# Performance work log

Hardware: AMD Instinct MI355X
Metric: run time of the kernel (lower is better)

Reference implementation:

```python
import jax, jax.numpy as jnp
import numpy as np

N_NODES = 100000


def setup_inputs() -> dict:
    key = jax.random.key(0)
    ks = jax.random.split(key, 8)
    IN, HID, OUT = 128, 128, 64
    E = 1600000
    x = jax.random.normal(ks[0], (N_NODES, IN), dtype=jnp.float32)
    edge_index = jax.random.randint(ks[1], (2, E), 0, N_NODES, dtype=jnp.int64)
    # PyG SAGEConv params: lin_l (applied to aggregated neighbors, with bias),
    # lin_r (root weight, no bias).
    def lin(k, fi, fo):
        return jax.random.normal(k, (fi, fo), dtype=jnp.float32) / np.sqrt(fi)
    Wl0 = lin(ks[2], IN, HID)
    bl0 = jnp.zeros((HID,), dtype=jnp.float32)
    Wr0 = lin(ks[3], IN, HID)
    Wl1 = lin(ks[4], HID, OUT)
    bl1 = jnp.zeros((OUT,), dtype=jnp.float32)
    Wr1 = lin(ks[5], HID, OUT)
    return {"x": x, "edge_index": edge_index,
            "Wl0": Wl0, "bl0": bl0, "Wr0": Wr0,
            "Wl1": Wl1, "bl1": bl1, "Wr1": Wr1}


def _sage_conv(h, src, dst, Wl, bl, Wr):
    # mean aggregation of source features onto target nodes
    summed = jax.ops.segment_sum(h[src], dst, num_segments=N_NODES)  # [N, d]
    cnt = jax.ops.segment_sum(jnp.ones((src.shape[0], 1), h.dtype), dst,
                              num_segments=N_NODES)                  # [N, 1]
    agg = summed / jnp.maximum(cnt, 1.0)
    return agg @ Wl + bl + h @ Wr


def reference(x, edge_index, Wl0, bl0, Wr0, Wl1, bl1, Wr1):
    src, dst = edge_index[0], edge_index[1]
    h = jax.nn.relu(_sage_conv(x, src, dst, Wl0, bl0, Wr0))
    # dropout is identity in eval mode (training=False)
    return _sage_conv(h, src, dst, Wl1, bl1, Wr1)
```

## Files before the change

### kernel.cpp

```cpp
#include <hip/hip_runtime.h>


typedef short short8 __attribute__((ext_vector_type(8)));
typedef float f32x4 __attribute__((ext_vector_type(4)));
typedef float f32x2 __attribute__((ext_vector_type(2)));

#define NBUCK 782
#define BCAP  3072
#define EPB   8192

static __device__ __forceinline__ unsigned short f2bf(float f) {
    union { float f; unsigned u; } c; c.f = f;
    unsigned u = c.u + 0x7fffu + ((c.u >> 16) & 1u);
    return (unsigned short)(u >> 16);
}
static __device__ __forceinline__ float bf2f(unsigned short b) {
    union { unsigned u; float f; } c; c.u = ((unsigned)b) << 16;
    return c.f;
}
static __device__ __forceinline__ float bf2f_s(short b) {
    return bf2f((unsigned short)b);
}

static __device__ __forceinline__ unsigned char f2fp8(float x) {
    union { float f; unsigned u; } c; c.f = x;
    unsigned s = (c.u >> 24) & 0x80u;
    float a = __builtin_fabsf(x);
    if (a < 0.015625f) {
        int m = (int)rintf(a * 512.0f);
        return (unsigned char)(s | (unsigned)m);
    }
    unsigned u = c.u + 0x7ffffu + ((c.u >> 20) & 1u);
    int e = (int)((u >> 23) & 0xff) - 120;
    unsigned m = (u >> 20) & 7u;
    if (e > 15) { e = 15; m = 6; }
    return (unsigned char)(s | (unsigned)(e << 3) | m);
}

static __device__ __forceinline__ void acc_fp8x4(unsigned w, float* a) {
#if __has_builtin(__builtin_amdgcn_cvt_pk_f32_fp8)
    f32x2 lo = __builtin_amdgcn_cvt_pk_f32_fp8((int)w, false);
    f32x2 hi = __builtin_amdgcn_cvt_pk_f32_fp8((int)w, true);
    a[0] += lo[0]; a[1] += lo[1]; a[2] += hi[0]; a[3] += hi[1];
#else
    #pragma unroll
    for (int j = 0; j < 4; ++j) {
        unsigned b = (w >> (8 * j)) & 0xffu;
        union { unsigned u; float f; } c;
        c.u = ((b & 0x80u) << 24) | ((b & 0x7fu) << 20);
        a[j] += c.f * 0x1p120f;
    }
#endif
}
static __device__ __forceinline__ void acc_row16(uint4 w, float* a) {
    acc_fp8x4(w.x, a + 0);  acc_fp8x4(w.y, a + 4);
    acc_fp8x4(w.z, a + 8);  acc_fp8x4(w.w, a + 12);
}

__global__ __launch_bounds__(256) void k_pack2(const float* __restrict__ Wl0,
        const float* __restrict__ Wr0, const float* __restrict__ Wl1,
        const float* __restrict__ Wr1, unsigned short* __restrict__ Wp0,
        unsigned short* __restrict__ Wp1) {
    int tid = blockIdx.x * 256 + threadIdx.x;
    const float *WA, *WB; int CA; unsigned short* Wp;
    if (tid < 4096) {
        WA = Wl0; WB = Wr0; CA = 128; Wp = Wp0;
    } else {
        tid -= 4096;
        if (tid >= 2048) return;
        WA = Wl1; WB = Wr1; CA = 64; Wp = Wp1;
    }
    int lane = tid & 63, kk = (tid >> 6) & 3, tg = tid >> 8;
    int l15 = lane & 15, quad = lane >> 4;
    int c = tg * 16 + l15;
    const float* W = (c < CA) ? WA : WB;
    int cc = (c < CA) ? c : c - CA;
    short8 v;
    #pragma unroll
    for (int j = 0; j < 8; ++j) {
        int k = kk * 32 + quad * 8 + j;
        v[j] = (short)f2bf(W[(size_t)k * CA + cc]);
    }
    *(short8*)(Wp + (size_t)tid * 8) = v;
}

__global__ __launch_bounds__(512) void k_gemm0_bucket(
        const float* __restrict__ X, const unsigned short* __restrict__ Wp,
        unsigned char* __restrict__ P0, unsigned short* __restrict__ Q0, int Nrows,
        const int* __restrict__ src, const int* __restrict__ dst,
        int* __restrict__ cursor, int* __restrict__ bregion,
        int E, int bucketBlocks) {
    const int t = threadIdx.x;
    if ((int)blockIdx.x >= bucketBlocks) {
        const int wave = t >> 6, lane = t & 63;
        const int sub = wave >> 2, wv = wave & 3;
        const int quad = lane >> 4, l15 = lane & 15;
        const int row0 = (blockIdx.x - bucketBlocks) * 64 + sub * 32;
        const int c0w = wv * 64;
        float4 xf[4][2][2];
        #pragma unroll
        for (int mt = 0; mt < 2; ++mt) {
            int row = row0 + mt * 16 + l15;
            if (row > Nrows - 1) row = Nrows - 1;
            const float* xp = X + (size_t)row * 128 + quad * 8;
            #pragma unroll
            for (int kk = 0; kk < 4; ++kk) {
                xf[kk][mt][0] = *(const float4*)(xp + kk * 32);
                xf[kk][mt][1] = *(const float4*)(xp + kk * 32 + 4);
            }
        }
        short8 a[4][2];
        #pragma unroll
        for (int kk = 0; kk < 4; ++kk)
            #pragma unroll
            for (int mt = 0; mt < 2; ++mt) {
                float4 f0 = xf[kk][mt][0], f1 = xf[kk][mt][1];
                short8 v;
                v[0] = (short)f2bf(f0.x); v[1] = (short)f2bf(f0.y);
                v[2] = (short)f2bf(f0.z); v[3] = (short)f2bf(f0.w);
                v[4] = (short)f2bf(f1.x); v[5] = (short)f2bf(f1.y);
                v[6] = (short)f2bf(f1.z); v[7] = (short)f2bf(f1.w);
                a[kk][mt] = v;
            }
        f32x4 acc[2][4];
        #pragma unroll
        for (int mt = 0; mt < 2; ++mt)
            #pragma unroll
            for (int tt = 0; tt < 4; ++tt) acc[mt][tt] = (f32x4){0.f, 0.f, 0.f, 0.f};
        #pragma unroll
        for (int kk = 0; kk < 4; ++kk) {
            short8 b[4];
            #pragma unroll
            for (int tt = 0; tt < 4; ++tt) {
                int tg = (c0w >> 4) + tt;
                b[tt] = *(const short8*)(Wp + ((size_t)(tg * 4 + kk) * 64 + lane) * 8);
            }
            #pragma unroll
            for (int mt = 0; mt < 2; ++mt)
                #pragma unroll
                for (int tt = 0; tt < 4; ++tt)
                    acc[mt][tt] = __builtin_amdgcn_mfma_f32_16x16x32_bf16(
                        a[kk][mt], b[tt], acc[mt][tt], 0, 0, 0);
        }
        #pragma unroll
        for (int mt = 0; mt < 2; ++mt)
            #pragma unroll
            for (int r = 0; r < 4; ++r) {
                int row = row0 + mt * 16 + quad * 4 + r;
                if (row < Nrows) {
                    if (c0w < 128) {
                        #pragma unroll
                        for (int tt = 0; tt < 4; ++tt)
                            P0[(size_t)row * 128 + c0w + tt * 16 + l15] =
                                f2fp8(acc[mt][tt][r]);
                    } else {
                        #pragma unroll
                        for (int tt = 0; tt < 4; ++tt)
                            Q0[(size_t)row * 128 + (c0w - 128) + tt * 16 + l15] =
                                f2bf(acc[mt][tt][r]);
                    }
                }
            }
        return;
    }
    __shared__ int hist[NBUCK];
    __shared__ int basel[NBUCK];
    int bid = blockIdx.x;
    for (int i = t; i < NBUCK; i += 512) hist[i] = 0;
    __syncthreads();
    int e0 = bid * EPB + t * 16;
    if (e0 + 16 <= E) {
        #pragma unroll
        for (int q = 0; q < 4; ++q) {
            int4 v = *(const int4*)(dst + e0 + q * 4);
            atomicAdd(&hist[v.x >> 7], 1);
            atomicAdd(&hist[v.y >> 7], 1);
            atomicAdd(&hist[v.z >> 7], 1);
            atomicAdd(&hist[v.w >> 7], 1);
        }
    } else {
        for (int j = 0; j < 16; ++j)
            if (e0 + j < E) atomicAdd(&hist[dst[e0 + j] >> 7], 1);
    }
    __syncthreads();
    for (int i = t; i < NBUCK; i += 512) {
        int c = hist[i];
        basel[i] = (c > 0) ? atomicAdd(&cursor[i], c) : 0;
    }
    __syncthreads();
    for (int i = t; i < NBUCK; i += 512) hist[i] = 0;
    __syncthreads();
    if (e0 + 16 <= E) {
        #pragma unroll
        for (int q = 0; q < 4; ++q) {
            int4 dv = *(const int4*)(dst + e0 + q * 4);
            int4 sv = *(const int4*)(src + e0 + q * 4);
            int dd[4] = {dv.x, dv.y, dv.z, dv.w};
            int ss[4] = {sv.x, sv.y, sv.z, sv.w};
            #pragma unroll
            for (int j = 0; j < 4; ++j) {
                int b = dd[j] >> 7;
                int r = atomicAdd(&hist[b], 1);
                bregion[(size_t)b * BCAP + basel[b] + r] = ss[j] | ((dd[j] & 127) << 20);
            }
        }
    } else {
        for (int j = 0; j < 16; ++j) {
            if (e0 + j < E) {
                int dd = dst[e0 + j], ss = src[e0 + j];
                int b = dd >> 7;
                int r = atomicAdd(&hist[b], 1);
                bregion[(size_t)b * BCAP + basel[b] + r] = ss | ((dd & 127) << 20);
            }
        }
    }
}

__global__ __launch_bounds__(256) void k_csr(const int* __restrict__ cursor,
                                             const int* __restrict__ bregion,
                                             int* __restrict__ rowptr,
                                             int* __restrict__ csr, int Nn) {
    __shared__ int words[BCAP];
    __shared__ int hist[128], sc[128], rank[128];
    __shared__ int red[256];
    int b = blockIdx.x, t = threadIdx.x;
    int part = 0;
    for (int i = t; i < b; i += 256) part += cursor[i];
    red[t] = part;
    if (t < 128) { hist[t] = 0; rank[t] = 0; }
    __syncthreads();
    #pragma unroll
    for (int off = 128; off > 0; off >>= 1) {
        if (t < off) red[t] += red[t + off];
        __syncthreads();
    }
    int gbase = red[0];
    int cnt = cursor[b];
    for (int i = t; i < cnt; i += 256) {
        int w = bregion[(size_t)b * BCAP + i];
        words[i] = w;
        atomicAdd(&hist[w >> 20], 1);
    }
    __syncthreads();
    if (t < 128) sc[t] = hist[t];
    __syncthreads();
    #pragma unroll
    for (int off = 1; off < 128; off <<= 1) {
        int x = 0;
        if (t < 128 && t >= off) x = sc[t - off];
        __syncthreads();
        if (t < 128) sc[t] += x;
        __syncthreads();
    }
    if (t < 128) sc[t] -= hist[t];
    __syncthreads();
    if (t < 128) {
        int node = b * 128 + t;
        if (node <= Nn) rowptr[node] = gbase + sc[t];
    }
    for (int i = t; i < cnt; i += 256) {
        int w = words[i];
        int d7 = w >> 20;
        int r = atomicAdd(&rank[d7], 1);
        csr[gbase + sc[d7] + r] = w & 0xFFFFF;
    }
}

__global__ __launch_bounds__(256) void k_agg0_gemm1(
        const unsigned char* __restrict__ P0,
        const unsigned short* __restrict__ Q0,
        const int* __restrict__ rowptr, const int* __restrict__ csr,
        const float* __restrict__ bl0,
        const unsigned short* __restrict__ Wp,
        unsigned char* __restrict__ P1, unsigned short* __restrict__ Q1,
        int Nn) {
    __shared__ unsigned short ht[32 * 128];
    const int t = threadIdx.x;
    const int wave = t >> 6, lane = t & 63;
    {
        int g = lane >> 3, l7 = lane & 7;
        int nloc = wave * 8 + g;
        int n = blockIdx.x * 32 + nloc;
        bool live = (n < Nn);
        int st = 0, dg = 0;
        if (live) { st = rowptr[n]; dg = rowptr[n + 1] - st; }
        float acc[16] = {};
        int e = 0;
        for (; e + 4 <= dg; e += 4) {
            int s0 = csr[st + e];
            int s1 = csr[st + e + 1];
            int s2 = csr[st + e + 2];
            int s3 = csr[st + e + 3];
            uint4 w0 = *(const uint4*)(P0 + (size_t)s0 * 128 + l7 * 16);
            uint4 w1 = *(const uint4*)(P0 + (size_t)s1 * 128 + l7 * 16);
            uint4 w2 = *(const uint4*)(P0 + (size_t)s2 * 128 + l7 * 16);
            uint4 w3 = *(const uint4*)(P0 + (size_t)s3 * 128 + l7 * 16);
            acc_row16(w0, acc);
            acc_row16(w1, acc);
            acc_row16(w2, acc);
            acc_row16(w3, acc);
        }
        for (; e < dg; ++e) {
            int s0 = csr[st + e];
            uint4 w0 = *(const uint4*)(P0 + (size_t)s0 * 128 + l7 * 16);
            acc_row16(w0, acc);
        }
        short8 o0 = (short8){0,0,0,0,0,0,0,0}, o1 = o0;
        if (live) {
            float inv = 1.f / fmaxf((float)dg, 1.f);
            short8 q0 = *(const short8*)(Q0 + (size_t)n * 128 + l7 * 16);
            short8 q1 = *(const short8*)(Q0 + (size_t)n * 128 + l7 * 16 + 8);
            float bb[16];
            *(float4*)(bb + 0)  = *(const float4*)(bl0 + l7 * 16);
            *(float4*)(bb + 4)  = *(const float4*)(bl0 + l7 * 16 + 4);
            *(float4*)(bb + 8)  = *(const float4*)(bl0 + l7 * 16 + 8);
            *(float4*)(bb + 12) = *(const float4*)(bl0 + l7 * 16 + 12);
            #pragma unroll
            for (int j = 0; j < 8; ++j)
                o0[j] = (short)f2bf(fmaxf(acc[j] * inv + bb[j] + bf2f_s(q0[j]), 0.f));
            #pragma unroll
            for (int j = 0; j < 8; ++j)
                o1[j] = (short)f2bf(fmaxf(acc[8 + j] * inv + bb[8 + j] + bf2f_s(q1[j]), 0.f));
        }
        unsigned sw = (unsigned)(nloc & 7) << 4;
        char* base = (char*)ht + nloc * 256;
        *(short8*)(base + (((unsigned)(l7 * 32)) ^ sw)) = o0;
        *(short8*)(base + (((unsigned)(l7 * 32 + 16)) ^ sw)) = o1;
    }
    __syncthreads();
    const int quad = lane >> 4, l15 = lane & 15;
    const int row0 = blockIdx.x * 32;
    const int c0w = wave * 32;
    f32x4 acc[2][2];
    #pragma unroll
    for (int mt = 0; mt < 2; ++mt)
        #pragma unroll
        for (int tt = 0; tt < 2; ++tt) acc[mt][tt] = (f32x4){0.f, 0.f, 0.f, 0.f};
    #pragma unroll
    for (int kk = 0; kk < 4; ++kk) {
        short8 a[2];
        #pragma unroll
        for (int mt = 0; mt < 2; ++mt) {
            int row = mt * 16 + l15;
            const char* p = (const char*)ht + row * 256 +
                (((unsigned)(kk * 64 + quad * 16)) ^ ((unsigned)(row & 7) << 4));
            a[mt] = *(const short8*)p;
        }
        short8 b[2];
        #pragma unroll
        for (int tt = 0; tt < 2; ++tt) {
            int tg = (c0w >> 4) + tt;
            b[tt] = *(const short8*)(Wp + ((size_t)(tg * 4 + kk) * 64 + lane) * 8);
        }
        #pragma unroll
        for (int mt = 0; mt < 2; ++mt)
            #pragma unroll
            for (int tt = 0; tt < 2; ++tt)
                acc[mt][tt] = __builtin_amdgcn_mfma_f32_16x16x32_bf16(
                    a[mt], b[tt], acc[mt][tt], 0, 0, 0);
    }
    #pragma unroll
    for (int mt = 0; mt < 2; ++mt)
        #pragma unroll
        for (int r = 0; r < 4; ++r) {
            int row = row0 + mt * 16 + quad * 4 + r;
            if (row < Nn) {
                if (c0w < 64) {
                    #pragma unroll
                    for (int tt = 0; tt < 2; ++tt)
                        P1[(size_t)row * 64 + c0w + tt * 16 + l15] =
                            f2fp8(acc[mt][tt][r]);
                } else {
                    #pragma unroll
                    for (int tt = 0; tt < 2; ++tt)
                        Q1[(size_t)row * 64 + (c0w - 64) + tt * 16 + l15] =
                            f2bf(acc[mt][tt][r]);
                }
            }
        }
}

__global__ __launch_bounds__(256) void k_agg1(const unsigned char* __restrict__ P1,
                                              const unsigned short* __restrict__ Q1,
                                              const int* __restrict__ rowptr,
                                              const int* __restrict__ csr,
                                              const float* __restrict__ bl1,
                                              float* __restrict__ out, int Nn) {
    int wave = threadIdx.x >> 6, lane = threadIdx.x & 63;
    int g = lane >> 2, l3 = lane & 3;
    int n = (blockIdx.x * 4 + wave) * 16 + g;
    bool live = (n < Nn);
    int st = 0, dg = 0;
    if (live) { st = rowptr[n]; dg = rowptr[n + 1] - st; }
    float acc[16] = {};
    int e = 0;
    for (; e + 4 <= dg; e += 4) {
        int s0 = csr[st + e];
        int s1 = csr[st + e + 1];
        int s2 = csr[st + e + 2];
        int s3 = csr[st + e + 3];
        uint4 w0 = *(const uint4*)(P1 + (size_t)s0 * 64 + l3 * 16);
        uint4 w1 = *(const uint4*)(P1 + (size_t)s1 * 64 + l3 * 16);
        uint4 w2 = *(const uint4*)(P1 + (size_t)s2 * 64 + l3 * 16);
        uint4 w3 = *(const uint4*)(P1 + (size_t)s3 * 64 + l3 * 16);
        acc_row16(w0, acc);
        acc_row16(w1, acc);
        acc_row16(w2, acc);
        acc_row16(w3, acc);
    }
    for (; e < dg; ++e) {
        int s0 = csr[st + e];
        uint4 w0 = *(const uint4*)(P1 + (size_t)s0 * 64 + l3 * 16);
        acc_row16(w0, acc);
    }
    if (live) {
        float inv = 1.f / fmaxf((float)dg, 1.f);
        short8 q0 = *(const short8*)(Q1 + (size_t)n * 64 + l3 * 16);
        short8 q1 = *(const short8*)(Q1 + (size_t)n * 64 + l3 * 16 + 8);
        float bb[16];
        *(float4*)(bb + 0)  = *(const float4*)(bl1 + l3 * 16);
        *(float4*)(bb + 4)  = *(const float4*)(bl1 + l3 * 16 + 4);
        *(float4*)(bb + 8)  = *(const float4*)(bl1 + l3 * 16 + 8);
        *(float4*)(bb + 12) = *(const float4*)(bl1 + l3 * 16 + 12);
        float4 o[4];
        #pragma unroll
        for (int j = 0; j < 8; ++j)
            ((float*)o)[j] = acc[j] * inv + bb[j] + bf2f_s(q0[j]);
        #pragma unroll
        for (int j = 0; j < 8; ++j)
            ((float*)o)[8 + j] = acc[8 + j] * inv + bb[8 + j] + bf2f_s(q1[j]);
        #pragma unroll
        for (int q = 0; q < 4; ++q)
            *(float4*)(out + (size_t)n * 64 + l3 * 16 + q * 4) = o[q];
    }
}

extern "C" void kernel_launch(void* const* d_in, const int* in_sizes, int n_in,
                              void* d_out, int out_size, void* d_ws, size_t ws_size,
                              hipStream_t stream) {
    const float* x   = (const float*)d_in[0];
    const int* eidx  = (const int*)d_in[1];
    const float* Wl0 = (const float*)d_in[2];
    const float* bl0 = (const float*)d_in[3];
    const float* Wr0 = (const float*)d_in[4];
    const float* Wl1 = (const float*)d_in[5];
    const float* bl1 = (const float*)d_in[6];
    const float* Wr1 = (const float*)d_in[7];
    float* out = (float*)d_out;

    const int N = in_sizes[0] / 128;
    const int E = in_sizes[1] / 2;
    const int* src = eidx;
    const int* dst = eidx + E;

    int* rowptr  = (int*)d_ws;
    int* cursor  = rowptr + (N + 4);
    int* bregion = cursor + 784;
    int* csr     = bregion + (size_t)NBUCK * BCAP;
    unsigned short* Wp0 = (unsigned short*)(csr + E);
    unsigned short* Wp1 = Wp0 + 32768;
    unsigned char*  P0  = (unsigned char*)(Wp1 + 16384);
    unsigned short* Q0  = (unsigned short*)(P0 + (size_t)N * 128);
    unsigned char*  P1  = (unsigned char*)(Q0 + (size_t)N * 128);
    unsigned short* Q1  = (unsigned short*)(P1 + (size_t)N * 64);

    hipMemsetAsync(cursor, 0, NBUCK * sizeof(int), stream);

    k_pack2<<<24, 256, 0, stream>>>(Wl0, Wr0, Wl1, Wr1, Wp0, Wp1);

    int gemmBlocks = (N + 63) / 64;
    int nbb = (E + EPB - 1) / EPB;
    k_gemm0_bucket<<<gemmBlocks + nbb, 512, 0, stream>>>(
        x, Wp0, P0, Q0, N, src, dst, cursor, bregion, E, nbb);
    k_csr<<<NBUCK, 256, 0, stream>>>(cursor, bregion, rowptr, csr, N);

    k_agg0_gemm1<<<(N + 31) / 32, 256, 0, stream>>>(
        P0, Q0, rowptr, csr, bl0, Wp1, P1, Q1, N);
    k_agg1<<<(N + 63) / 64, 256, 0, stream>>>(P1, Q1, rowptr, csr, bl1, out, N);
}
```

Before: 277.7 us.

## Slice P1 into column-major feature slices and split layer-1 aggregation by slice

P1 (the fp8 layer-1 projections) is now stored as four separate 16-column slices, each contiguous across nodes, instead of 64-byte rows. The layer-1 aggregation launches four times as many blocks, each handling one 16-column slice. The four lanes that share a node now split that node's edge list and combine their partial sums with xor shuffles. This shrinks the gathered working set per slice to improve cache hit rates and spreads edges across lanes. The cost is four re-reads of the CSR and rowptr data, plus the shuffle reduction.

```diff
diff --git a/kernel.cpp b/kernel.cpp
--- a/kernel.cpp
+++ b/kernel.cpp
@@ -367,9 +367,11 @@
             if (row < Nn) {
                 if (c0w < 64) {
                     #pragma unroll
-                    for (int tt = 0; tt < 2; ++tt)
-                        P1[(size_t)row * 64 + c0w + tt * 16 + l15] =
-                            f2fp8(acc[mt][tt][r]);
+                    for (int tt = 0; tt < 2; ++tt) {
+                        int slice = (c0w >> 4) + tt;
+                        P1[(size_t)slice * ((size_t)Nn * 16) +
+                           (size_t)row * 16 + l15] = f2fp8(acc[mt][tt][r]);
+                    }
                 } else {
                     #pragma unroll
                     for (int tt = 0; tt < 2; ++tt)
@@ -386,53 +388,56 @@
                                               const int* __restrict__ csr,
                                               const float* __restrict__ bl1,
                                               float* __restrict__ out, int Nn) {
-    int wave = threadIdx.x >> 6, lane = threadIdx.x & 63;
-    int g = lane >> 2, l3 = lane & 3;
-    int n = (blockIdx.x * 4 + wave) * 16 + g;
-    bool live = (n < Nn);
-    int st = 0, dg = 0;
-    if (live) { st = rowptr[n]; dg = rowptr[n + 1] - st; }
+    const int t = threadIdx.x;
+    const int wave = t >> 6, lane = t & 63;
+    const int l3 = lane & 3;
+    const int g = wave * 16 + (lane >> 2);
+    const int s = blockIdx.x & 3;
+    const int n = (blockIdx.x >> 2) * 64 + g;
+    if (n >= Nn) return;
+    const unsigned char* Ps = P1 + (size_t)s * ((size_t)Nn * 16);
+    int st = rowptr[n], dg = rowptr[n + 1] - st;
     float acc[16] = {};
-    int e = 0;
-    for (; e + 4 <= dg; e += 4) {
+    int e = l3;
+    for (; e + 4 < dg; e += 8) {
         int s0 = csr[st + e];
-        int s1 = csr[st + e + 1];
-        int s2 = csr[st + e + 2];
-        int s3 = csr[st + e + 3];
-        uint4 w0 = *(const uint4*)(P1 + (size_t)s0 * 64 + l3 * 16);
-        uint4 w1 = *(const uint4*)(P1 + (size_t)s1 * 64 + l3 * 16);
-        uint4 w2 = *(const uint4*)(P1 + (size_t)s2 * 64 + l3 * 16);
-        uint4 w3 = *(const uint4*)(P1 + (size_t)s3 * 64 + l3 * 16);
+        int s1 = csr[st + e + 4];
+        uint4 w0 = *(const uint4*)(Ps + (size_t)s0 * 16);
+        uint4 w1 = *(const uint4*)(Ps + (size_t)s1 * 16);
         acc_row16(w0, acc);
         acc_row16(w1, acc);
-        acc_row16(w2, acc);
-        acc_row16(w3, acc);
-    }
-    for (; e < dg; ++e) {
+    }
+    if (e < dg) {
         int s0 = csr[st + e];
-        uint4 w0 = *(const uint4*)(P1 + (size_t)s0 * 64 + l3 * 16);
+        uint4 w0 = *(const uint4*)(Ps + (size_t)s0 * 16);
         acc_row16(w0, acc);
     }
-    if (live) {
-        float inv = 1.f / fmaxf((float)dg, 1.f);
-        short8 q0 = *(const short8*)(Q1 + (size_t)n * 64 + l3 * 16);
-        short8 q1 = *(const short8*)(Q1 + (size_t)n * 64 + l3 * 16 + 8);
-        float bb[16];
-        *(float4*)(bb + 0)  = *(const float4*)(bl1 + l3 * 16);
-        *(float4*)(bb + 4)  = *(const float4*)(bl1 + l3 * 16 + 4);
-        *(float4*)(bb + 8)  = *(const float4*)(bl1 + l3 * 16 + 8);
-        *(float4*)(bb + 12) = *(const float4*)(bl1 + l3 * 16 + 12);
-        float4 o[4];
-        #pragma unroll
-        for (int j = 0; j < 8; ++j)
-            ((float*)o)[j] = acc[j] * inv + bb[j] + bf2f_s(q0[j]);
-        #pragma unroll
-        for (int j = 0; j < 8; ++j)
-            ((float*)o)[8 + j] = acc[8 + j] * inv + bb[8 + j] + bf2f_s(q1[j]);
-        #pragma unroll
-        for (int q = 0; q < 4; ++q)
-            *(float4*)(out + (size_t)n * 64 + l3 * 16 + q * 4) = o[q];
-    }
+    bool hi1 = (l3 & 1) != 0;
+    float r1[8];
+    #pragma unroll
+    for (int j = 0; j < 8; ++j) {
+        float mine   = hi1 ? acc[8 + j] : acc[j];
+        float theirs = hi1 ? acc[j]     : acc[8 + j];
+        r1[j] = mine + __shfl_xor(theirs, 1);
+    }
+    bool hi2 = (l3 & 2) != 0;
+    float r2[4];
+    #pragma unroll
+    for (int j = 0; j < 4; ++j) {
+        float mine   = hi2 ? r1[4 + j] : r1[j];
+        float theirs = hi2 ? r1[j]     : r1[4 + j];
+        r2[j] = mine + __shfl_xor(theirs, 2);
+    }
+    int cb = (l3 & 1) * 8 + (l3 & 2) * 2;
+    float inv = 1.f / fmaxf((float)dg, 1.f);
+    ushort4 qv = *(const ushort4*)(Q1 + (size_t)n * 64 + s * 16 + cb);
+    float4 bb = *(const float4*)(bl1 + s * 16 + cb);
+    float4 o;
+    o.x = r2[0] * inv + bb.x + bf2f(qv.x);
+    o.y = r2[1] * inv + bb.y + bf2f(qv.y);
+    o.z = r2[2] * inv + bb.z + bf2f(qv.z);
+    o.w = r2[3] * inv + bb.w + bf2f(qv.w);
+    *(float4*)(out + (size_t)n * 64 + s * 16 + cb) = o;
 }
 
 extern "C" void kernel_launch(void* const* d_in, const int* in_sizes, int n_in,
@@ -476,5 +481,6 @@
 
     k_agg0_gemm1<<<(N + 31) / 32, 256, 0, stream>>>(
         P0, Q0, rowptr, csr, bl0, Wp1, P1, Q1, N);
-    k_agg1<<<(N + 63) / 64, 256, 0, stream>>>(P1, Q1, rowptr, csr, bl1, out, N);
-}
+    k_agg1<<<4 * ((N + 63) / 64), 256, 0, stream>>>(
+        P1, Q1, rowptr, csr, bl1, out, N);
+}
```

Result: no change. 281.5 us (+1.4%).
